# Kernel optimization log

Hardware: AMD Instinct MI355X
Metric: run time of the kernel (lower is better)

## Reference

```python
import jax, jax.numpy as jnp
import numpy as np


def setup_inputs() -> dict:
    key = jax.random.key(0)
    ks = jax.random.split(key, 7)
    B, C, H, W = 8, 256, 64, 64
    Cp = C // 8
    sc = 1.0 / np.sqrt(C)
    return {
        "x": jax.random.normal(ks[0], (B, C, H, W), dtype=jnp.float32),
        "Wq": jax.random.normal(ks[1], (Cp, C), dtype=jnp.float32) * sc,
        "bq": jnp.zeros((Cp,), dtype=jnp.float32),
        "Wk": jax.random.normal(ks[2], (Cp, C), dtype=jnp.float32) * sc,
        "bk": jnp.zeros((Cp,), dtype=jnp.float32),
        "Wv": jax.random.normal(ks[3], (C, C), dtype=jnp.float32) * sc,
        "bv": jnp.zeros((C,), dtype=jnp.float32),
        "gamma": jnp.float32(0.5),
    }


def reference(x, Wq, bq, Wk, bk, Wv, bv, gamma):
    B, C, H, W = x.shape
    xf = x.reshape(B, C, H * W)                         # (B, C, N)
    # 1x1 Conv1d == per-position linear over channels
    q = jnp.einsum('dc,bcn->bnd', Wq, xf) + bq          # (B, N, Cp)
    k = jnp.einsum('dc,bcn->bdn', Wk, xf) + bk[:, None] # (B, Cp, N)
    v = jnp.einsum('dc,bcn->bdn', Wv, xf) + bv[:, None] # (B, C, N)
    scores = jnp.einsum('bnd,bdm->bnm', q, k)           # (B, N, N)
    attn = jax.nn.softmax(scores, axis=-1)              # (B, N, N)
    # o = v @ attn^T : o[:, :, n] = sum_m attn[n, m] * v[:, :, m]
    o = jnp.einsum('bcm,bnm->bcn', v, attn)             # (B, C, N)
    o = o.reshape(B, C, H, W)
    return gamma * o + x
```

## Files before the change

### kernel.cpp

```cpp
#include <hip/hip_runtime.h>
#include <hip/hip_bf16.h>


constexpr int C  = 256;
constexpr int CP = 32;
constexpr int NPOS = 4096;
constexpr int NB = 8;
constexpr int MT = 64;
constexpr int NT = NPOS / MT;
constexpr float LOG2E = 1.44269504088896340736f;

typedef __attribute__((ext_vector_type(4))) float  f32x4;
typedef __attribute__((ext_vector_type(4))) short  bf16x4;
typedef __attribute__((ext_vector_type(8))) short  bf16x8;

__device__ __forceinline__ void bar_lds() {
    asm volatile("s_waitcnt lgkmcnt(0)\n\ts_barrier" ::: "memory");
}
__device__ __forceinline__ void wait_vm0() {
    asm volatile("s_waitcnt vmcnt(0)" ::: "memory");
}
__device__ __forceinline__ void wait_vm4() {
    asm volatile("s_waitcnt vmcnt(4)" ::: "memory");
}
__device__ __forceinline__ void wait_vm1() {
    asm volatile("s_waitcnt vmcnt(1)" ::: "memory");
}
__device__ __forceinline__ void gl_lds16(const void* gsrc, void* ldst) {
    typedef const __attribute__((address_space(1))) void* gp_t;
    typedef __attribute__((address_space(3))) void* lp_t;
    __builtin_amdgcn_global_load_lds((gp_t)gsrc, (lp_t)ldst, 16, 0, 0);
}
__device__ __forceinline__ short f2bf(float f) {
    __hip_bfloat16 h = __float2bfloat16(f);
    return __builtin_bit_cast(short, h);
}
__device__ __forceinline__ float ex2(float f) {
    return __builtin_amdgcn_exp2f(f);
}
__device__ __forceinline__ f32x4 mfma16(bf16x8 a, bf16x8 b, f32x4 c) {
    return __builtin_amdgcn_mfma_f32_16x16x32_bf16(a, b, c, 0, 0, 0);
}

__global__ __launch_bounds__(256) void wprep_kernel(
    const float* __restrict__ Wq, const float* __restrict__ bq,
    const float* __restrict__ Wk, const float* __restrict__ bk,
    const float* __restrict__ Wv, const float* __restrict__ bv,
    __hip_bfloat16* __restrict__ wh, __hip_bfloat16* __restrict__ wl,
    float* __restrict__ bcat)
{
    const int r = blockIdx.x, c = threadIdx.x;
    float w;
    if (r < 32)      w = Wq[r * 256 + c];
    else if (r < 64) w = Wk[(r - 32) * 256 + c];
    else             w = Wv[(r - 64) * 256 + c];
    __hip_bfloat16 h = __float2bfloat16(w);
    wh[r * 256 + c] = h;
    wl[r * 256 + c] = __float2bfloat16(w - __bfloat162float(h));
    if (c == 0)
        bcat[r] = (r < 32) ? bq[r] : (r < 64) ? bk[r - 32] : bv[r - 64];
}

__global__ __launch_bounds__(256) void xtrans_kernel(
    const float* __restrict__ x, __hip_bfloat16* __restrict__ xT)
{
    __shared__ float xl[64][65];
    const int tid = threadIdx.x;
    const int b   = blockIdx.x >> 8;
    const int rem = blockIdx.x & 255;
    const int c0  = (rem >> 6) << 6;
    const int n0  = (rem & 63) << 6;

    const float* xb = x + ((size_t)b * C + c0) * NPOS + n0;
    #pragma unroll
    for (int k = 0; k < 4; ++k) {
        const int idx = tid + k * 256;
        const int c = idx >> 4, j4 = idx & 15;
        float4 gg = *reinterpret_cast<const float4*>(xb + (size_t)c * NPOS + j4 * 4);
        xl[c][j4 * 4 + 0] = gg.x; xl[c][j4 * 4 + 1] = gg.y;
        xl[c][j4 * 4 + 2] = gg.z; xl[c][j4 * 4 + 3] = gg.w;
    }
    __syncthreads();

    const int nl = tid >> 2, cseg = tid & 3;
    bf16x8 o0, o1;
    #pragma unroll
    for (int j = 0; j < 8; ++j) {
        o0[j] = f2bf(xl[cseg * 16 + j][nl]);
        o1[j] = f2bf(xl[cseg * 16 + 8 + j][nl]);
    }
    __hip_bfloat16* dst = xT + ((size_t)b * NPOS + n0 + nl) * C + c0 + cseg * 16;
    *reinterpret_cast<bf16x8*>(dst)     = o0;
    *reinterpret_cast<bf16x8*>(dst + 8) = o1;
}

__global__ __launch_bounds__(512)
__attribute__((amdgpu_waves_per_eu(4)))
void qkv_mfma_kernel(
    const __hip_bfloat16* __restrict__ xT,
    const __hip_bfloat16* __restrict__ wh, const __hip_bfloat16* __restrict__ wl,
    const float* __restrict__ bcat,
    __hip_bfloat16* __restrict__ qh, __hip_bfloat16* __restrict__ ql,
    __hip_bfloat16* __restrict__ kh, __hip_bfloat16* __restrict__ kl,
    __hip_bfloat16* __restrict__ vT)
{
    __shared__ __align__(16) __hip_bfloat16 xlds[16384];
    __shared__ __align__(16) __hip_bfloat16 wlds[3][4096];

    const int tid = threadIdx.x;
    const int b  = blockIdx.x & 7;
    const int n0 = (blockIdx.x >> 3) << 6;
    const int l  = tid & 63;
    const int g  = tid >> 6;
    const int G  = l >> 4;
    const int li = l & 15;
    const int cs = g >> 1, ns0 = (g & 1) * 2;

    #pragma unroll
    for (int j = 0; j < 4; ++j)
        gl_lds16(xT + ((size_t)b * NPOS + n0 + l) * C + (j * 8 + g) * 8,
                 xlds + (j * 512 + g * 64) * 8);

    auto stageW = [&](int t, int d) {
        const int ct = t >> 3, ks = t & 7;
        const __hip_bfloat16* src = (g < 4) ? wh : wl;
        const int gg = g & 3;
        gl_lds16(src + (size_t)(ct * 64 + l) * 256 + ks * 32 + gg * 8,
                 &wlds[d][((g >= 4) ? 2048 : 0) + gg * 512]);
    };
    stageW(0, 0);
    stageW(1, 1);

    f32x4 acc0 = (f32x4){0.f, 0.f, 0.f, 0.f};
    f32x4 acc1 = (f32x4){0.f, 0.f, 0.f, 0.f};

    for (int t = 0; t < 40; ++t) {
        wait_vm1();
        bar_lds();
        if (t + 2 < 40) stageW(t + 2, (t + 2) % 3);

        const int ks = t & 7;
        const __hip_bfloat16* wb = wlds[t % 3];
        bf16x8 whf = *reinterpret_cast<const bf16x8*>(wb + (G * 64 + cs * 16 + li) * 8);
        bf16x8 wlf = *reinterpret_cast<const bf16x8*>(wb + 2048 + (G * 64 + cs * 16 + li) * 8);
        bf16x8 xf0 = *reinterpret_cast<const bf16x8*>(
            xlds + (ks * 256 + G * 64 + ns0 * 16 + li) * 8);
        bf16x8 xf1 = *reinterpret_cast<const bf16x8*>(
            xlds + (ks * 256 + G * 64 + (ns0 + 1) * 16 + li) * 8);
        acc0 = mfma16(whf, xf0, acc0);
        acc0 = mfma16(wlf, xf0, acc0);
        acc1 = mfma16(whf, xf1, acc1);
        acc1 = mfma16(wlf, xf1, acc1);

        if (ks == 7) {
            const int ct = t >> 3;
            const int cb = ct * 64 + cs * 16 + G * 4;
            const float4 b4 = *reinterpret_cast<const float4*>(bcat + cb);
            const float bb[4] = {b4.x, b4.y, b4.z, b4.w};
            #pragma unroll
            for (int j = 0; j < 2; ++j) {
                const f32x4 a = j ? acc1 : acc0;
                const int n_abs = n0 + (ns0 + j) * 16 + li;
                if (ct == 0) {
                    __hip_bfloat16* hb = (cs < 2) ? qh : kh;
                    __hip_bfloat16* lb = (cs < 2) ? ql : kl;
                    const float qsc = (cs < 2) ? LOG2E : 1.0f;
                    const int cq = (cs < 2) ? cb : cb - 32;
                    const size_t base = ((size_t)b * NPOS + n_abs) * CP + cq;
                    #pragma unroll
                    for (int r = 0; r < 4; ++r) {
                        const float val = (a[r] + bb[r]) * qsc;
                        __hip_bfloat16 h = __float2bfloat16(val);
                        hb[base + r] = h;
                        lb[base + r] = __float2bfloat16(val - __bfloat162float(h));
                    }
                } else {
                    const int cv = cb - 64;
                    #pragma unroll
                    for (int r = 0; r < 4; ++r)
                        vT[((size_t)b * C + cv + r) * NPOS + n_abs] =
                            __float2bfloat16(a[r] + bb[r]);
                }
            }
            acc0 = (f32x4){0.f, 0.f, 0.f, 0.f};
            acc1 = (f32x4){0.f, 0.f, 0.f, 0.f};
        }
    }
}

__global__ __launch_bounds__(512)
__attribute__((amdgpu_waves_per_eu(4)))
void attn_kernel(
    const __hip_bfloat16* __restrict__ qh, const __hip_bfloat16* __restrict__ ql,
    const __hip_bfloat16* __restrict__ kh, const __hip_bfloat16* __restrict__ kl,
    const __hip_bfloat16* __restrict__ vT, const float* __restrict__ x,
    const float* __restrict__ gamma_p, float* __restrict__ out)
{
    __shared__ __align__(16) __hip_bfloat16 k_lds[2][2][2048];
    __shared__ __align__(16) __hip_bfloat16 p_lds[2][4096];
    __shared__ float psm[2][64];

    const int tid = threadIdx.x;
    const int b  = blockIdx.x & 7;
    const int qt = blockIdx.x >> 3;
    const int l  = tid & 63;
    const int g  = tid >> 6;
    const int G  = l >> 4;
    const int li = l & 15;
    const int nj = g & 3, gr = g >> 2;
    const int mi0 = gr * 2;
    const int sn = nj * 16 + li;

    const __hip_bfloat16* khb = kh + (size_t)b * NPOS * CP;
    const __hip_bfloat16* klb = kl + (size_t)b * NPOS * CP;
    const __hip_bfloat16* vTb = vT + (size_t)b * C * NPOS;

    bf16x8 qhf, qlf;
    {
        const size_t qoff = ((size_t)b * NPOS + qt * 64 + nj * 16 + li) * CP + G * 8;
        qhf = *reinterpret_cast<const bf16x8*>(qh + qoff);
        qlf = *reinterpret_cast<const bf16x8*>(ql + qoff);
    }

    const __hip_bfloat16* vp0 = vTb + (size_t)(g * 32 + li) * NPOS + G * 8;
    const __hip_bfloat16* vp1 = vTb + (size_t)(g * 32 + 16 + li) * NPOS + G * 8;

    f32x4 acc[4][2];
    #pragma unroll
    for (int nt = 0; nt < 4; ++nt)
        #pragma unroll
        for (int ct = 0; ct < 2; ++ct) acc[nt][ct] = (f32x4){0.f, 0.f, 0.f, 0.f};
    float lsum_reg = 0.f;

    auto stageK = [&](int tt, int bufd) {
        const __hip_bfloat16* ks = (gr == 0) ? khb : klb;
        gl_lds16(ks + (size_t)tt * MT * CP + l * CP + nj * 8,
                 &k_lds[bufd][gr][nj * 512]);
    };
    auto qkp = [&](int tt) {
        const int bufq = tt & 1;
        const int kfo = (G * 64 + mi0 * 16 + li) * 8;
        bf16x8 kh0 = *reinterpret_cast<const bf16x8*>(&k_lds[bufq][0][kfo]);
        bf16x8 kl0 = *reinterpret_cast<const bf16x8*>(&k_lds[bufq][1][kfo]);
        bf16x8 kh1 = *reinterpret_cast<const bf16x8*>(&k_lds[bufq][0][kfo + 128]);
        bf16x8 kl1 = *reinterpret_cast<const bf16x8*>(&k_lds[bufq][1][kfo + 128]);
        f32x4 s0 = (f32x4){0.f, 0.f, 0.f, 0.f};
        s0 = mfma16(kh0, qhf, s0); s0 = mfma16(kh0, qlf, s0); s0 = mfma16(kl0, qhf, s0);
        f32x4 s1 = (f32x4){0.f, 0.f, 0.f, 0.f};
        s1 = mfma16(kh1, qhf, s1); s1 = mfma16(kh1, qlf, s1); s1 = mfma16(kl1, qhf, s1);
        float p0[4], p1[4];
        #pragma unroll
        for (int r = 0; r < 4; ++r) {
            p0[r] = ex2(s0[r]);
            p1[r] = ex2(s1[r]);
        }
        lsum_reg += ((p0[0] + p0[1]) + (p0[2] + p0[3]))
                  + ((p1[0] + p1[1]) + (p1[2] + p1[3]));
        const int ms0 = mi0 * 4 + G;
        bf16x4 w0 = { f2bf(p0[0]), f2bf(p0[1]), f2bf(p0[2]), f2bf(p0[3]) };
        *reinterpret_cast<bf16x4*>(&p_lds[bufq][ms0 * 256 + ((sn ^ ms0) * 4)]) = w0;
        const int ms1 = ms0 + 4;
        bf16x4 w1 = { f2bf(p1[0]), f2bf(p1[1]), f2bf(p1[2]), f2bf(p1[3]) };
        *reinterpret_cast<bf16x4*>(&p_lds[bufq][ms1 * 256 + ((sn ^ ms1) * 4)]) = w1;
    };
    auto pv = [&](int tt, const bf16x8 vf[4]) {
        const __hip_bfloat16* pb = p_lds[tt & 1];
        #pragma unroll
        for (int s = 0; s < 2; ++s) {
            const bf16x8 af0 = vf[s];
            const bf16x8 af1 = vf[2 + s];
            bf16x8 bfr[4];
            #pragma unroll
            for (int nt = 0; nt < 4; ++nt) {
                const int n = nt * 16 + li;
                const int ma = s * 8 + 2 * G, mb = ma + 1;
                bf16x4 blo = *reinterpret_cast<const bf16x4*>(
                    pb + ma * 256 + ((n ^ ma) * 4));
                bf16x4 bhi = *reinterpret_cast<const bf16x4*>(
                    pb + mb * 256 + ((n ^ mb) * 4));
                bfr[nt] = __builtin_shufflevector(blo, bhi, 0,1,2,3,4,5,6,7);
            }
            #pragma unroll
            for (int nt = 0; nt < 4; ++nt) {
                acc[nt][0] = mfma16(af0, bfr[nt], acc[nt][0]);
                acc[nt][1] = mfma16(af1, bfr[nt], acc[nt][1]);
            }
        }
    };

    bf16x8 vcur[4], vnxt[4];

    stageK(0, 0);
    stageK(1, 1);
    vcur[0] = *reinterpret_cast<const bf16x8*>(vp0);
    vcur[1] = *reinterpret_cast<const bf16x8*>(vp0 + 32);
    vcur[2] = *reinterpret_cast<const bf16x8*>(vp1);
    vcur[3] = *reinterpret_cast<const bf16x8*>(vp1 + 32);
    wait_vm0();
    bar_lds();
    qkp(0);
    bar_lds();

    for (int t = 0; t < NT - 1; ++t) {
        stageK((t + 2) & (NT - 1), t & 1);
        __builtin_amdgcn_sched_barrier(0);
        {
            const __hip_bfloat16* q0 = vp0 + (t + 1) * MT;
            const __hip_bfloat16* q1 = vp1 + (t + 1) * MT;
            vnxt[0] = *reinterpret_cast<const bf16x8*>(q0);
            vnxt[1] = *reinterpret_cast<const bf16x8*>(q0 + 32);
            vnxt[2] = *reinterpret_cast<const bf16x8*>(q1);
            vnxt[3] = *reinterpret_cast<const bf16x8*>(q1 + 32);
        }
        __builtin_amdgcn_sched_barrier(0);

        __builtin_amdgcn_s_setprio(1);
        qkp(t + 1);
        pv(t, vcur);
        __builtin_amdgcn_s_setprio(0);

        wait_vm4();
        bar_lds();
        #pragma unroll
        for (int i = 0; i < 4; ++i) vcur[i] = vnxt[i];
    }
    pv(NT - 1, vcur);

    float ps = lsum_reg;
    ps += __shfl_xor(ps, 16);
    ps += __shfl_xor(ps, 32);
    if (G == 0) psm[gr][sn] = ps;
    bar_lds();

    const float gamma = *gamma_p;
    const float* xb = x   + (size_t)b * C * NPOS;
    float*       ob = out + (size_t)b * C * NPOS;

    #pragma unroll
    for (int nt = 0; nt < 4; ++nt) {
        const int cidx = nt * 16 + li;
        const float inv = 1.0f / (psm[0][cidx] + psm[1][cidx]);
        const int n = qt * 64 + cidx;
        #pragma unroll
        for (int ct = 0; ct < 2; ++ct) {
            const int c0 = g * 32 + ct * 16 + G * 4;
            #pragma unroll
            for (int r = 0; r < 4; ++r) {
                const size_t idx = (size_t)(c0 + r) * NPOS + n;
                ob[idx] = gamma * acc[nt][ct][r] * inv + xb[idx];
            }
        }
    }
}

extern "C" void kernel_launch(void* const* d_in, const int* in_sizes, int n_in,
                              void* d_out, int out_size, void* d_ws, size_t ws_size,
                              hipStream_t stream) {
    const float* x  = (const float*)d_in[0];
    const float* Wq = (const float*)d_in[1];
    const float* bq = (const float*)d_in[2];
    const float* Wk = (const float*)d_in[3];
    const float* bk = (const float*)d_in[4];
    const float* Wv = (const float*)d_in[5];
    const float* bv = (const float*)d_in[6];
    const float* gamma = (const float*)d_in[7];
    float* out = (float*)d_out;

    const size_t qk_n = (size_t)NB * NPOS * CP;
    const size_t v_n  = (size_t)NB * C * NPOS;
    __hip_bfloat16* qhb = (__hip_bfloat16*)d_ws;
    __hip_bfloat16* qlb = qhb + qk_n;
    __hip_bfloat16* khb = qlb + qk_n;
    __hip_bfloat16* klb = khb + qk_n;
    __hip_bfloat16* vT  = klb + qk_n;
    __hip_bfloat16* xT  = vT + v_n;
    __hip_bfloat16* wh  = xT + v_n;
    __hip_bfloat16* wl  = wh + 320 * 256;
    float*          bcat = (float*)(wl + 320 * 256);

    xtrans_kernel<<<NB * 4 * 64, 256, 0, stream>>>(x, xT);
    wprep_kernel<<<320, 256, 0, stream>>>(Wq, bq, Wk, bk, Wv, bv, wh, wl, bcat);
    qkv_mfma_kernel<<<NB * (NPOS / 64), 512, 0, stream>>>(xT, wh, wl, bcat,
                                                          qhb, qlb, khb, klb, vT);
    attn_kernel<<<NB * (NPOS / 64), 512, 0, stream>>>(qhb, qlb, khb, klb, vT,
                                                      x, gamma, out);
}
```

Baseline: 185.5 us.

## Transpose P tile in LDS with XOR swizzle and unroll loop by two

Stores the probability tile row-per-query with a 16-byte XOR swizzle, so the PV step reads one 128-bit LDS load per fragment instead of two 64-bit loads plus a shuffle. The main loop is manually unrolled by two with ping-pong V registers and compile-time buffer indices. This removes the vcur/vnxt register copies and the dynamic buffer indexing. It also adds an explicit tail iteration, which raises code size and the risk of mistakes in prefetch indexing.

```diff
diff --git a/kernel.cpp b/kernel.cpp
--- a/kernel.cpp
+++ b/kernel.cpp
@@ -197,7 +197,7 @@
     const float* __restrict__ gamma_p, float* __restrict__ out)
 {
     __shared__ __align__(16) __hip_bfloat16 k_lds[2][2][2048];
-    __shared__ __align__(16) __hip_bfloat16 p_lds[2][4096];
+    __shared__ __align__(16) __hip_bfloat16 p_lds[2][64][64];
     __shared__ float psm[2][64];
 
     const int tid = threadIdx.x;
@@ -210,6 +210,7 @@
     const int nj = g & 3, gr = g >> 2;
     const int mi0 = gr * 2;
     const int sn = nj * 16 + li;
+    const int swz = (li & 7) << 4;
 
     const __hip_bfloat16* khb = kh + (size_t)b * NPOS * CP;
     const __hip_bfloat16* klb = kl + (size_t)b * NPOS * CP;
@@ -237,13 +238,12 @@
         gl_lds16(ks + (size_t)tt * MT * CP + l * CP + nj * 8,
                  &k_lds[bufd][gr][nj * 512]);
     };
-    auto qkp = [&](int tt) {
-        const int bufq = tt & 1;
+    auto qkp = [&](int PB) {
         const int kfo = (G * 64 + mi0 * 16 + li) * 8;
-        bf16x8 kh0 = *reinterpret_cast<const bf16x8*>(&k_lds[bufq][0][kfo]);
-        bf16x8 kl0 = *reinterpret_cast<const bf16x8*>(&k_lds[bufq][1][kfo]);
-        bf16x8 kh1 = *reinterpret_cast<const bf16x8*>(&k_lds[bufq][0][kfo + 128]);
-        bf16x8 kl1 = *reinterpret_cast<const bf16x8*>(&k_lds[bufq][1][kfo + 128]);
+        bf16x8 kh0 = *reinterpret_cast<const bf16x8*>(&k_lds[PB][0][kfo]);
+        bf16x8 kl0 = *reinterpret_cast<const bf16x8*>(&k_lds[PB][1][kfo]);
+        bf16x8 kh1 = *reinterpret_cast<const bf16x8*>(&k_lds[PB][0][kfo + 128]);
+        bf16x8 kl1 = *reinterpret_cast<const bf16x8*>(&k_lds[PB][1][kfo + 128]);
         f32x4 s0 = (f32x4){0.f, 0.f, 0.f, 0.f};
         s0 = mfma16(kh0, qhf, s0); s0 = mfma16(kh0, qlf, s0); s0 = mfma16(kl0, qhf, s0);
         f32x4 s1 = (f32x4){0.f, 0.f, 0.f, 0.f};
@@ -256,75 +256,81 @@
         }
         lsum_reg += ((p0[0] + p0[1]) + (p0[2] + p0[3]))
                   + ((p1[0] + p1[1]) + (p1[2] + p1[3]));
-        const int ms0 = mi0 * 4 + G;
+        char* prow = reinterpret_cast<char*>(&p_lds[PB][0][0]) + sn * 128;
         bf16x4 w0 = { f2bf(p0[0]), f2bf(p0[1]), f2bf(p0[2]), f2bf(p0[3]) };
-        *reinterpret_cast<bf16x4*>(&p_lds[bufq][ms0 * 256 + ((sn ^ ms0) * 4)]) = w0;
-        const int ms1 = ms0 + 4;
+        *reinterpret_cast<bf16x4*>(prow + ((gr * 64 + G * 8) ^ swz)) = w0;
         bf16x4 w1 = { f2bf(p1[0]), f2bf(p1[1]), f2bf(p1[2]), f2bf(p1[3]) };
-        *reinterpret_cast<bf16x4*>(&p_lds[bufq][ms1 * 256 + ((sn ^ ms1) * 4)]) = w1;
-    };
-    auto pv = [&](int tt, const bf16x8 vf[4]) {
-        const __hip_bfloat16* pb = p_lds[tt & 1];
+        *reinterpret_cast<bf16x4*>(prow + ((gr * 64 + 32 + G * 8) ^ swz)) = w1;
+    };
+    auto pv = [&](int PB, const bf16x8 vf[4]) {
+        const char* pb = reinterpret_cast<const char*>(&p_lds[PB][0][0]);
         #pragma unroll
         for (int s = 0; s < 2; ++s) {
             const bf16x8 af0 = vf[s];
             const bf16x8 af1 = vf[2 + s];
-            bf16x8 bfr[4];
             #pragma unroll
             for (int nt = 0; nt < 4; ++nt) {
-                const int n = nt * 16 + li;
-                const int ma = s * 8 + 2 * G, mb = ma + 1;
-                bf16x4 blo = *reinterpret_cast<const bf16x4*>(
-                    pb + ma * 256 + ((n ^ ma) * 4));
-                bf16x4 bhi = *reinterpret_cast<const bf16x4*>(
-                    pb + mb * 256 + ((n ^ mb) * 4));
-                bfr[nt] = __builtin_shufflevector(blo, bhi, 0,1,2,3,4,5,6,7);
-            }
-            #pragma unroll
-            for (int nt = 0; nt < 4; ++nt) {
-                acc[nt][0] = mfma16(af0, bfr[nt], acc[nt][0]);
-                acc[nt][1] = mfma16(af1, bfr[nt], acc[nt][1]);
+                const bf16x8 bfr = *reinterpret_cast<const bf16x8*>(
+                    pb + (nt * 16 + li) * 128 + ((s * 64 + G * 16) ^ swz));
+                acc[nt][0] = mfma16(af0, bfr, acc[nt][0]);
+                acc[nt][1] = mfma16(af1, bfr, acc[nt][1]);
             }
         }
     };
-
-    bf16x8 vcur[4], vnxt[4];
+    auto loadV = [&](bf16x8 vf[4], int tt) {
+        const __hip_bfloat16* q0 = vp0 + tt * MT;
+        const __hip_bfloat16* q1 = vp1 + tt * MT;
+        vf[0] = *reinterpret_cast<const bf16x8*>(q0);
+        vf[1] = *reinterpret_cast<const bf16x8*>(q0 + 32);
+        vf[2] = *reinterpret_cast<const bf16x8*>(q1);
+        vf[3] = *reinterpret_cast<const bf16x8*>(q1 + 32);
+    };
+
+    bf16x8 vA[4], vB[4];
 
     stageK(0, 0);
     stageK(1, 1);
-    vcur[0] = *reinterpret_cast<const bf16x8*>(vp0);
-    vcur[1] = *reinterpret_cast<const bf16x8*>(vp0 + 32);
-    vcur[2] = *reinterpret_cast<const bf16x8*>(vp1);
-    vcur[3] = *reinterpret_cast<const bf16x8*>(vp1 + 32);
+    loadV(vA, 0);
     wait_vm0();
     bar_lds();
     qkp(0);
     bar_lds();
 
-    for (int t = 0; t < NT - 1; ++t) {
-        stageK((t + 2) & (NT - 1), t & 1);
+    #pragma unroll 1
+    for (int tp = 0; tp < 31; ++tp) {
+        const int t = tp * 2;
+        stageK(t + 2, 0);
         __builtin_amdgcn_sched_barrier(0);
-        {
-            const __hip_bfloat16* q0 = vp0 + (t + 1) * MT;
-            const __hip_bfloat16* q1 = vp1 + (t + 1) * MT;
-            vnxt[0] = *reinterpret_cast<const bf16x8*>(q0);
-            vnxt[1] = *reinterpret_cast<const bf16x8*>(q0 + 32);
-            vnxt[2] = *reinterpret_cast<const bf16x8*>(q1);
-            vnxt[3] = *reinterpret_cast<const bf16x8*>(q1 + 32);
-        }
+        loadV(vB, t + 1);
         __builtin_amdgcn_sched_barrier(0);
-
         __builtin_amdgcn_s_setprio(1);
-        qkp(t + 1);
-        pv(t, vcur);
+        qkp(1);
+        pv(0, vA);
         __builtin_amdgcn_s_setprio(0);
-
         wait_vm4();
         bar_lds();
-        #pragma unroll
-        for (int i = 0; i < 4; ++i) vcur[i] = vnxt[i];
-    }
-    pv(NT - 1, vcur);
+        stageK(t + 3, 1);
+        __builtin_amdgcn_sched_barrier(0);
+        loadV(vA, t + 2);
+        __builtin_amdgcn_sched_barrier(0);
+        __builtin_amdgcn_s_setprio(1);
+        qkp(0);
+        pv(1, vB);
+        __builtin_amdgcn_s_setprio(0);
+        wait_vm4();
+        bar_lds();
+    }
+    stageK(0, 0);
+    __builtin_amdgcn_sched_barrier(0);
+    loadV(vB, 63);
+    __builtin_amdgcn_sched_barrier(0);
+    __builtin_amdgcn_s_setprio(1);
+    qkp(1);
+    pv(0, vA);
+    __builtin_amdgcn_s_setprio(0);
+    wait_vm4();
+    bar_lds();
+    pv(1, vB);
 
     float ps = lsum_reg;
     ps += __shfl_xor(ps, 16);
```

After: 185.4 us. About the same (-0.1%).
